# Performance work log

Hardware: AMD Instinct MI355X
Metric: run time of the kernel (lower is better)

Reference implementation:

```python
import jax, jax.numpy as jnp
import numpy as np

B, W, NN, EPG = 8, 16, 64, 1024   # batch, window, nodes/graph, trace-edges/graph
N = B * W * NN                     # 8192 flattened nodes
E = B * W * EPG                    # 131072 node-graph edges == trace rows
E2 = 4 * E                         # 524288 edge-graph (line-graph) edges
D_NODE = 128; D_LOG = 128; D_EDGE = 128
D_IN = D_NODE + D_LOG              # 256 = GATv2 node2node in_channels
H = 4
EPS = 1e-16                        # PyG softmax epsilon


def _lin(key, fan_in, fan_out):
    return jax.random.normal(key, (fan_in, fan_out), jnp.float32) * (1.0 / np.sqrt(fan_in))


def setup_inputs() -> dict:
    key = jax.random.key(0)
    ks = jax.random.split(key, 16)
    return {
        "x_node": jax.random.normal(ks[0], (B, W, NN, D_NODE), jnp.float32),
        "x_trace": jax.random.normal(ks[1], (B, W, EPG, D_EDGE), jnp.float32),
        "x_log": jax.random.normal(ks[2], (B, W, NN, D_LOG), jnp.float32),
        "node_adj": jax.random.randint(ks[3], (2, E), 0, N, jnp.int32),
        "edge_adj": jax.random.randint(ks[4], (2, E2), 0, E, jnp.int32),
        "edge_efea": jax.random.randint(ks[5], (E2,), 0, N, jnp.int32),
        # node2node GATv2Conv: in=256, heads=4, out/head=64, edge_dim=128
        "n2n_Wl": _lin(ks[6], D_IN, D_IN), "n2n_bl": jnp.zeros((D_IN,), jnp.float32),
        "n2n_Wr": _lin(ks[7], D_IN, D_IN), "n2n_br": jnp.zeros((D_IN,), jnp.float32),
        "n2n_We": _lin(ks[8], D_EDGE, D_IN),
        "n2n_att": jax.random.normal(ks[9], (H, D_IN // H), jnp.float32) * 0.1,
        "n2n_bias": jnp.zeros((D_IN,), jnp.float32),
        # egde2node GATv2Conv: in=128, heads=4, out/head=32, edge_dim=256
        "e2n_Wl": _lin(ks[10], D_EDGE, D_EDGE), "e2n_bl": jnp.zeros((D_EDGE,), jnp.float32),
        "e2n_Wr": _lin(ks[11], D_EDGE, D_EDGE), "e2n_br": jnp.zeros((D_EDGE,), jnp.float32),
        "e2n_We": _lin(ks[12], D_IN, D_EDGE),
        "e2n_att": jax.random.normal(ks[13], (H, D_EDGE // H), jnp.float32) * 0.1,
        "e2n_bias": jnp.zeros((D_EDGE,), jnp.float32),
    }


def gatv2(x, edge_index, edge_attr, Wl, bl, Wr, br, We, att, bias, num_nodes):
    """PyG GATv2Conv (eval mode, add_self_loops=False, concat heads)."""
    heads, C = att.shape
    src, dst = edge_index[0], edge_index[1]
    xl = (x @ Wl + bl).reshape(-1, heads, C)   # source transform [N,H,C]
    xr = (x @ Wr + br).reshape(-1, heads, C)   # target transform [N,H,C]
    e = (edge_attr @ We).reshape(-1, heads, C) # edge transform   [E,H,C]
    m = jax.nn.leaky_relu(xl[src] + xr[dst] + e, 0.2)  # [E,H,C]
    alpha = jnp.einsum('ehc,hc->eh', m, att)           # [E,H]
    amax = jax.ops.segment_max(alpha, dst, num_segments=num_nodes)
    ex = jnp.exp(alpha - amax[dst])
    denom = jax.ops.segment_sum(ex, dst, num_segments=num_nodes)
    a = ex / (denom[dst] + EPS)                        # per-target softmax
    out = jax.ops.segment_sum(a[:, :, None] * xl[src], dst, num_segments=num_nodes)
    return out.reshape(num_nodes, heads * C) + bias


def reference(x_node, x_trace, x_log, node_adj, edge_adj, edge_efea,
              n2n_Wl, n2n_bl, n2n_Wr, n2n_br, n2n_We, n2n_att, n2n_bias,
              e2n_Wl, e2n_bl, e2n_Wr, e2n_br, e2n_We, e2n_att, e2n_bias):
    node = jnp.concatenate([x_node, x_log], axis=-1).reshape(-1, D_IN)  # [N,256]
    trace = x_trace.reshape(-1, D_EDGE)                                 # [E,128]
    node = gatv2(node, node_adj, trace,
                 n2n_Wl, n2n_bl, n2n_Wr, n2n_br, n2n_We, n2n_att, n2n_bias, N)
    trace = gatv2(trace, edge_adj, node[edge_efea],
                  e2n_Wl, e2n_bl, e2n_Wr, e2n_br, e2n_We, e2n_att, e2n_bias, E)
    xn = node[:, :D_NODE].reshape(B, W, NN, D_NODE)
    xt = trace.reshape(B, W, EPG, D_EDGE)
    xlg = node[:, D_NODE:].reshape(B, W, NN, D_LOG)
    return (xn, xt, xlg)
```

## Files before the change

### kernel.cpp

```cpp
#include <hip/hip_runtime.h>
#include <hip/hip_bf16.h>

constexpr int N    = 8192;
constexpr int E    = 131072;
constexpr int E2   = 524288;

constexpr size_t XT_OFF  = (size_t)N * 128;
constexpr size_t XLG_OFF = XT_OFF + (size_t)E * 128;

typedef unsigned short u16;
typedef short s16x8 __attribute__((ext_vector_type(8)));
typedef float f32x4 __attribute__((ext_vector_type(4)));

__device__ __forceinline__ u16 f2bs(float f) {
    unsigned x = __float_as_uint(f);
    return (u16)((x + 0x7FFF + ((x >> 16) & 1)) >> 16);
}
__device__ __forceinline__ float bs2f(u16 u) {
    return __uint_as_float((unsigned)u << 16);
}

__global__ __launch_bounds__(256) void k_prep(
    const float* __restrict__ Wl, const float* __restrict__ Wr,
    const float* __restrict__ We, const float* __restrict__ Wl2,
    const float* __restrict__ Wr2, const float* __restrict__ We2,
    u16* __restrict__ Wlt, u16* __restrict__ Wrt, u16* __restrict__ Wet,
    u16* __restrict__ Wl2t, u16* __restrict__ Wr2t, u16* __restrict__ We2t)
{
    const int gid = blockIdx.x * 256 + threadIdx.x;
    const float* src; u16* dst; int base, Kk, sh;
    if      (gid <  65536) { src = Wl;  dst = Wlt;  base = 0;      Kk = 256; sh = 8; }
    else if (gid < 131072) { src = Wr;  dst = Wrt;  base = 65536;  Kk = 256; sh = 8; }
    else if (gid < 163840) { src = We;  dst = Wet;  base = 131072; Kk = 128; sh = 8; }
    else if (gid < 180224) { src = Wl2; dst = Wl2t; base = 163840; Kk = 128; sh = 7; }
    else if (gid < 196608) { src = Wr2; dst = Wr2t; base = 180224; Kk = 128; sh = 7; }
    else                   { src = We2; dst = We2t; base = 196608; Kk = 256; sh = 7; }
    const int l = gid - base;
    const int k = l >> sh, nn = l & ((1 << sh) - 1);
    dst[(size_t)nn * Kk + k] = f2bs(src[l]);
}

__global__ void k_hist(const int* __restrict__ dst, int* __restrict__ cnt, int nE)
{
    int i = blockIdx.x * 256 + threadIdx.x;
    if (i < nE) atomicAdd(&cnt[dst[i]], 1);
}

__global__ __launch_bounds__(1024) void k_scan(
    const int* __restrict__ cnt, int* __restrict__ off, int* __restrict__ cur, int n)
{
    __shared__ int tile[8192];
    __shared__ int wsum[16];
    const int tid = threadIdx.x, lane = tid & 63, wv = tid >> 6;
    int carry = 0;
    for (int base = 0; base < n; base += 8192) {
        for (int i = tid; i < 8192; i += 1024) tile[i] = cnt[base + i];
        __syncthreads();
        const int st = tid * 8;
        int s = 0;
        for (int k = 0; k < 8; ++k) { int v = tile[st + k]; tile[st + k] = s; s += v; }
        const int tsum = s;
        int incl = s;
        for (int o = 1; o < 64; o <<= 1) {
            int v = __shfl_up(incl, o);
            if (lane >= o) incl += v;
        }
        if (lane == 63) wsum[wv] = incl;
        __syncthreads();
        int woff = 0;
        for (int wq = 0; wq < wv; ++wq) woff += wsum[wq];
        int tot = 0;
        for (int wq = 0; wq < 16; ++wq) tot += wsum[wq];
        const int add = carry + woff + incl - tsum;
        for (int k = 0; k < 8; ++k) {
            int o2 = add + tile[st + k];
            off[base + st + k] = o2;
            cur[base + st + k] = o2;
        }
        carry += tot;
        __syncthreads();
    }
    if (tid == 0) off[n] = carry;
}

__global__ void k_scatter1(const int* __restrict__ adj, int* __restrict__ cur,
                           int* __restrict__ srcc, int* __restrict__ pos1, int nE)
{
    int i = blockIdx.x * 256 + threadIdx.x;
    if (i < nE) {
        int pos = atomicAdd(&cur[adj[nE + i]], 1);
        srcc[pos] = adj[i];
        pos1[i] = pos;
    }
}

__global__ void k_scatter2(const int* __restrict__ eadj, const int* __restrict__ efea,
                           int* __restrict__ cur, int2* __restrict__ sf2, int nE)
{
    int i = blockIdx.x * 256 + threadIdx.x;
    if (i < nE) {
        int pos = atomicAdd(&cur[eadj[nE + i]], 1);
        sf2[pos] = make_int2(eadj[i], efea[i]);
    }
}

__global__ __launch_bounds__(256) void k_node_gemm(
    const float* __restrict__ x_node, const float* __restrict__ x_log,
    const u16* __restrict__ Wlt, const float* __restrict__ bl,
    const u16* __restrict__ Wrt, const float* __restrict__ br,
    u16* __restrict__ xl, u16* __restrict__ xr)
{
    __shared__ u16 A[32][260];
    const int n0 = blockIdx.x * 32;
    const int tid = threadIdx.x;
    for (int i = tid; i < 32 * 64; i += 256) {
        const int r = i >> 6, k4 = (i & 63) << 2;
        const float* srcp = (k4 < 128) ? &x_node[(size_t)(n0 + r) * 128 + k4]
                                       : &x_log [(size_t)(n0 + r) * 128 + (k4 - 128)];
        const float4 v = *(const float4*)srcp;
        ushort4 o; o.x = f2bs(v.x); o.y = f2bs(v.y); o.z = f2bs(v.z); o.w = f2bs(v.w);
        *(ushort4*)&A[r][k4] = o;
    }
    __syncthreads();
    const int w = tid >> 6, lane = tid & 63, lr = lane & 15, lq = lane >> 4;
    const u16* Wt     = (w < 2) ? Wlt : Wrt;
    const float* bias = (w < 2) ? bl : br;
    u16* outp         = (w < 2) ? xl : xr;
    const int cb = (w & 1) * 128;
    f32x4 acc[2][8] = {};
    for (int kb = 0; kb < 8; ++kb) {
        s16x8 afr0 = *(const s16x8*)&A[lr][kb * 32 + lq * 8];
        s16x8 afr1 = *(const s16x8*)&A[16 + lr][kb * 32 + lq * 8];
#pragma unroll
        for (int ct = 0; ct < 8; ++ct) {
            const int n = cb + ct * 16 + lr;
            s16x8 bfr = *(const s16x8*)&Wt[(size_t)n * 256 + kb * 32 + lq * 8];
            acc[0][ct] = __builtin_amdgcn_mfma_f32_16x16x32_bf16(afr0, bfr, acc[0][ct], 0, 0, 0);
            acc[1][ct] = __builtin_amdgcn_mfma_f32_16x16x32_bf16(afr1, bfr, acc[1][ct], 0, 0, 0);
        }
    }
#pragma unroll
    for (int rt = 0; rt < 2; ++rt)
#pragma unroll
        for (int ct = 0; ct < 8; ++ct) {
            const int col = cb + ct * 16 + lr;
            const float bv = bias[col];
#pragma unroll
            for (int reg = 0; reg < 4; ++reg) {
                const int row = n0 + rt * 16 + lq * 4 + reg;
                outp[(size_t)row * 256 + col] = f2bs(acc[rt][ct][reg] + bv);
            }
        }
}

__global__ __launch_bounds__(256) void k_trace_gemm(
    const float* __restrict__ x_trace,
    const u16* __restrict__ Wl2t, const float* __restrict__ bl,
    const u16* __restrict__ Wr2t, const float* __restrict__ br,
    u16* __restrict__ xl, u16* __restrict__ xrst)
{
    __shared__ u16 A[32][132];
    const int e0 = blockIdx.x * 32;
    const int tid = threadIdx.x;
    for (int i = tid; i < 32 * 32; i += 256) {
        const int r = i >> 5, k4 = (i & 31) << 2;
        const float4 v = *(const float4*)&x_trace[(size_t)(e0 + r) * 128 + k4];
        ushort4 o; o.x = f2bs(v.x); o.y = f2bs(v.y); o.z = f2bs(v.z); o.w = f2bs(v.w);
        *(ushort4*)&A[r][k4] = o;
    }
    __syncthreads();
    const int w = tid >> 6, lane = tid & 63, lr = lane & 15, lq = lane >> 4;
    const u16* Wt     = (w < 2) ? Wl2t : Wr2t;
    const float* bias = (w < 2) ? bl : br;
    const int cb = (w & 1) * 64;
    f32x4 acc[2][4] = {};
    for (int kb = 0; kb < 4; ++kb) {
        s16x8 afr0 = *(const s16x8*)&A[lr][kb * 32 + lq * 8];
        s16x8 afr1 = *(const s16x8*)&A[16 + lr][kb * 32 + lq * 8];
#pragma unroll
        for (int ct = 0; ct < 4; ++ct) {
            const int n = cb + ct * 16 + lr;
            s16x8 bfr = *(const s16x8*)&Wt[(size_t)n * 128 + kb * 32 + lq * 8];
            acc[0][ct] = __builtin_amdgcn_mfma_f32_16x16x32_bf16(afr0, bfr, acc[0][ct], 0, 0, 0);
            acc[1][ct] = __builtin_amdgcn_mfma_f32_16x16x32_bf16(afr1, bfr, acc[1][ct], 0, 0, 0);
        }
    }
#pragma unroll
    for (int rt = 0; rt < 2; ++rt)
#pragma unroll
        for (int ct = 0; ct < 4; ++ct) {
            const int col = cb + ct * 16 + lr;
            const float bv = bias[col];
#pragma unroll
            for (int reg = 0; reg < 4; ++reg) {
                const int row = e0 + rt * 16 + lq * 4 + reg;
                if (w < 2) xl[(size_t)row * 128 + col]   = f2bs(acc[rt][ct][reg] + bv);
                else       xrst[(size_t)row * 256 + col] = f2bs(acc[rt][ct][reg] + bv);
            }
        }
}

__global__ __launch_bounds__(256) void k_edge_alpha1(
    const float* __restrict__ x_trace,
    const int* __restrict__ adj,
    const int* __restrict__ pos1,
    const u16* __restrict__ xl, const u16* __restrict__ xr,
    const u16* __restrict__ Wet, const float* __restrict__ att,
    float* __restrict__ alpha)
{
    __shared__ u16 A[32][132];
    __shared__ int ss[32], dd[32], pp[32];
    const int e0 = blockIdx.x * 32;
    const int tid = threadIdx.x;
    for (int i = tid; i < 32 * 32; i += 256) {
        const int r = i >> 5, k4 = (i & 31) << 2;
        const float4 v = *(const float4*)&x_trace[(size_t)(e0 + r) * 128 + k4];
        ushort4 o; o.x = f2bs(v.x); o.y = f2bs(v.y); o.z = f2bs(v.z); o.w = f2bs(v.w);
        *(ushort4*)&A[r][k4] = o;
    }
    if (tid < 32) {
        ss[tid] = adj[e0 + tid];
        dd[tid] = adj[E + e0 + tid];
        pp[tid] = pos1[e0 + tid];
    }
    __syncthreads();
    const int w = tid >> 6, lane = tid & 63, lr = lane & 15, lq = lane >> 4;
    f32x4 acc[2][4] = {};
    for (int kb = 0; kb < 4; ++kb) {
        s16x8 afr0 = *(const s16x8*)&A[lr][kb * 32 + lq * 8];
        s16x8 afr1 = *(const s16x8*)&A[16 + lr][kb * 32 + lq * 8];
#pragma unroll
        for (int ct = 0; ct < 4; ++ct) {
            const int n = w * 64 + ct * 16 + lr;
            s16x8 bfr = *(const s16x8*)&Wet[(size_t)n * 128 + kb * 32 + lq * 8];
            acc[0][ct] = __builtin_amdgcn_mfma_f32_16x16x32_bf16(afr0, bfr, acc[0][ct], 0, 0, 0);
            acc[1][ct] = __builtin_amdgcn_mfma_f32_16x16x32_bf16(afr1, bfr, acc[1][ct], 0, 0, 0);
        }
    }
    float attv[4];
#pragma unroll
    for (int ct = 0; ct < 4; ++ct) attv[ct] = att[w * 64 + ct * 16 + lr];
    float sums[2][4] = {};
#pragma unroll
    for (int rt = 0; rt < 2; ++rt)
#pragma unroll
        for (int reg = 0; reg < 4; ++reg) {
            const int rowt = rt * 16 + lq * 4 + reg;
            const int s = ss[rowt], d = dd[rowt];
            float acc_s = 0.f;
#pragma unroll
            for (int ct = 0; ct < 4; ++ct) {
                const int col = w * 64 + ct * 16 + lr;
                float m = acc[rt][ct][reg]
                        + bs2f(xl[(size_t)s * 256 + col])
                        + bs2f(xr[(size_t)d * 256 + col]);
                m = m > 0.f ? m : 0.2f * m;
                acc_s += m * attv[ct];
            }
            sums[rt][reg] = acc_s;
        }
#pragma unroll
    for (int rt = 0; rt < 2; ++rt)
#pragma unroll
        for (int reg = 0; reg < 4; ++reg) {
            float p = sums[rt][reg];
            p += __shfl_xor(p, 8);
            p += __shfl_xor(p, 4);
            p += __shfl_xor(p, 2);
            p += __shfl_xor(p, 1);
            if (lr == 0)
                alpha[(size_t)pp[rt * 16 + lq * 4 + reg] * 4 + w] = p;
        }
}

__global__ __launch_bounds__(256) void k_fused1(
    const int* __restrict__ off, const int* __restrict__ srcc,
    const float* __restrict__ alphac,
    const u16* __restrict__ xl,
    const float* __restrict__ bias,
    float* __restrict__ out)
{
    const int wv = __builtin_amdgcn_readfirstlane(threadIdx.x >> 6);
    const int lane = threadIdx.x & 63;
    const int n = blockIdx.x * 4 + wv;
    const int c = lane * 4;
    const int h = lane >> 4;
    const int beg = off[n], end = off[n + 1];
    float mx = -INFINITY, den = 0.f;
    float a0 = 0.f, a1 = 0.f, a2 = 0.f, a3 = 0.f;
    int i = beg;
    while (i < end) {
        const int rem = end - i;
        int sa[8]; float pe[8];
#pragma unroll
        for (int k = 0; k < 8; ++k) {
            const int idx = i + (k < rem ? k : rem - 1);
            sa[k] = srcc[idx];
            pe[k] = alphac[(size_t)idx * 4 + h];
        }
        ushort4 xv[8];
#pragma unroll
        for (int k = 0; k < 8; ++k)
            xv[k] = *(const ushort4*)&xl[(size_t)sa[k] * 256 + c];
#pragma unroll
        for (int k = 0; k < 8; ++k) {
            const float p = (k < rem) ? pe[k] : -INFINITY;
            const float mnew = fmaxf(mx, p);
            const float sc = __expf(mx - mnew);
            const float ex = __expf(p - mnew);
            den = den * sc + ex;
            a0 = a0 * sc + ex * bs2f(xv[k].x);
            a1 = a1 * sc + ex * bs2f(xv[k].y);
            a2 = a2 * sc + ex * bs2f(xv[k].z);
            a3 = a3 * sc + ex * bs2f(xv[k].w);
            mx = mnew;
        }
        i += 8;
    }
    const float inv = 1.f / (den + 1e-16f);
    float4 r;
    r.x = a0 * inv + bias[c + 0];
    r.y = a1 * inv + bias[c + 1];
    r.z = a2 * inv + bias[c + 2];
    r.w = a3 * inv + bias[c + 3];
    if (lane < 32) *(float4*)&out[(size_t)n * 128 + c] = r;
    else           *(float4*)&out[XLG_OFF + (size_t)n * 128 + (c - 128)] = r;
}

__global__ __launch_bounds__(256) void k_proj_gemm(
    const float* __restrict__ out_node, const u16* __restrict__ We2t,
    u16* __restrict__ proj)
{
    __shared__ u16 A[32][260];
    const int n0 = blockIdx.x * 32;
    const int tid = threadIdx.x;
    for (int i = tid; i < 32 * 64; i += 256) {
        const int r = i >> 6, k4 = (i & 63) << 2;
        const float* srcp = (k4 < 128)
            ? &out_node[(size_t)(n0 + r) * 128 + k4]
            : &out_node[XLG_OFF + (size_t)(n0 + r) * 128 + (k4 - 128)];
        const float4 v = *(const float4*)srcp;
        ushort4 o; o.x = f2bs(v.x); o.y = f2bs(v.y); o.z = f2bs(v.z); o.w = f2bs(v.w);
        *(ushort4*)&A[r][k4] = o;
    }
    __syncthreads();
    const int w = tid >> 6, lane = tid & 63, lr = lane & 15, lq = lane >> 4;
    f32x4 acc[2][2] = {};
    for (int kb = 0; kb < 8; ++kb) {
        s16x8 afr0 = *(const s16x8*)&A[lr][kb * 32 + lq * 8];
        s16x8 afr1 = *(const s16x8*)&A[16 + lr][kb * 32 + lq * 8];
#pragma unroll
        for (int ct = 0; ct < 2; ++ct) {
            const int col = w * 32 + ct * 16 + lr;
            s16x8 bfr = *(const s16x8*)&We2t[(size_t)col * 256 + kb * 32 + lq * 8];
            acc[0][ct] = __builtin_amdgcn_mfma_f32_16x16x32_bf16(afr0, bfr, acc[0][ct], 0, 0, 0);
            acc[1][ct] = __builtin_amdgcn_mfma_f32_16x16x32_bf16(afr1, bfr, acc[1][ct], 0, 0, 0);
        }
    }
#pragma unroll
    for (int rt = 0; rt < 2; ++rt)
#pragma unroll
        for (int ct = 0; ct < 2; ++ct) {
            const int col = w * 32 + ct * 16 + lr;
#pragma unroll
            for (int reg = 0; reg < 4; ++reg) {
                const int row = n0 + rt * 16 + lq * 4 + reg;
                proj[(size_t)row * 128 + col] = f2bs(acc[rt][ct][reg]);
            }
        }
}

__global__ __launch_bounds__(256) void k_fused2(
    const int* __restrict__ off, const int2* __restrict__ sf2,
    const u16* __restrict__ xl,
    const u16* __restrict__ proj,
    const float* __restrict__ att,
    const float* __restrict__ bias,
    float* __restrict__ out)
{
    const int wv = __builtin_amdgcn_readfirstlane(threadIdx.x >> 6);
    const int lane = threadIdx.x & 63;
    const int d = blockIdx.x * 4 + wv;
    const int c = lane * 2;
    const u16* xrst = (const u16*)(out + XT_OFF);
    const unsigned xrp = *(const unsigned*)&xrst[(size_t)d * 256 + c];
    const float xr0 = bs2f((u16)(xrp & 0xffff));
    const float xr1 = bs2f((u16)(xrp >> 16));
    const float av0 = att[c], av1 = att[c + 1];
    const int beg = off[d], end = off[d + 1];
    float mx = -INFINITY, den = 0.f, a0 = 0.f, a1 = 0.f;
    int i = beg;
    while (i < end) {
        const int rem = end - i;
        int2 sf[4];
#pragma unroll
        for (int k = 0; k < 4; ++k) sf[k] = sf2[i + (k < rem ? k : rem - 1)];
        unsigned xv[4], pv[4];
#pragma unroll
        for (int k = 0; k < 4; ++k) {
            xv[k] = *(const unsigned*)&xl[(size_t)sf[k].x * 128 + c];
            pv[k] = *(const unsigned*)&proj[(size_t)sf[k].y * 128 + c];
        }
#pragma unroll
        for (int k = 0; k < 4; ++k) {
            const float x0 = bs2f((u16)(xv[k] & 0xffff));
            const float x1 = bs2f((u16)(xv[k] >> 16));
            float m0 = x0 + xr0 + bs2f((u16)(pv[k] & 0xffff));
            float m1 = x1 + xr1 + bs2f((u16)(pv[k] >> 16));
            m0 = m0 > 0.f ? m0 : 0.2f * m0;
            m1 = m1 > 0.f ? m1 : 0.2f * m1;
            float pp = m0 * av0 + m1 * av1;
            pp += __shfl_xor(pp, 8, 16);
            pp += __shfl_xor(pp, 4, 16);
            pp += __shfl_xor(pp, 2, 16);
            pp += __shfl_xor(pp, 1, 16);
            const float p = (k < rem) ? pp : -INFINITY;
            const float mnew = fmaxf(mx, p);
            const float sc = __expf(mx - mnew);
            const float ex = __expf(p - mnew);
            den = den * sc + ex;
            a0 = a0 * sc + ex * x0;
            a1 = a1 * sc + ex * x1;
            mx = mnew;
        }
        i += 4;
    }
    const float inv = 1.f / (den + 1e-16f);
    float2 o2;
    o2.x = a0 * inv + bias[c];
    o2.y = a1 * inv + bias[c + 1];
    *(float2*)&out[XT_OFF + (size_t)d * 128 + c] = o2;
}

extern "C" void kernel_launch(void* const* d_in, const int* in_sizes, int n_in,
                              void* d_out, int out_size, void* d_ws, size_t ws_size,
                              hipStream_t stream)
{
    const float* x_node   = (const float*)d_in[0];
    const float* x_trace  = (const float*)d_in[1];
    const float* x_log    = (const float*)d_in[2];
    const int*   node_adj = (const int*)d_in[3];
    const int*   edge_adj = (const int*)d_in[4];
    const int*   efea     = (const int*)d_in[5];
    const float* n2n_Wl   = (const float*)d_in[6];
    const float* n2n_bl   = (const float*)d_in[7];
    const float* n2n_Wr   = (const float*)d_in[8];
    const float* n2n_br   = (const float*)d_in[9];
    const float* n2n_We   = (const float*)d_in[10];
    const float* n2n_att  = (const float*)d_in[11];
    const float* n2n_bias = (const float*)d_in[12];
    const float* e2n_Wl   = (const float*)d_in[13];
    const float* e2n_bl   = (const float*)d_in[14];
    const float* e2n_Wr   = (const float*)d_in[15];
    const float* e2n_br   = (const float*)d_in[16];
    const float* e2n_We   = (const float*)d_in[17];
    const float* e2n_att  = (const float*)d_in[18];
    const float* e2n_bias = (const float*)d_in[19];
    float* out = (float*)d_out;

    char* w = (char*)d_ws;
    int*  cnt1   = (int*)w;   w += (size_t)N * 4;
    int*  cnt2   = (int*)w;   w += (size_t)E * 4;
    int*  off1   = (int*)w;   w += (size_t)(N + 4) * 4;
    int*  cur1   = (int*)w;   w += (size_t)N * 4;
    int*  src1   = (int*)w;   w += (size_t)E * 4;
    int*  pos1   = (int*)w;   w += (size_t)E * 4;
    float* alphac = (float*)w; w += (size_t)E * 4 * 4;
    int*  off2   = (int*)w;   w += (size_t)(E + 4) * 4;
    int*  cur2   = (int*)w;   w += (size_t)E * 4;
    int2* sf2    = (int2*)w;  w += (size_t)E2 * 8;
    u16*  xl_n   = (u16*)w;   w += (size_t)N * 256 * 2;
    u16*  xr_n   = (u16*)w;   w += (size_t)N * 256 * 2;
    u16*  xl_e   = (u16*)w;   w += (size_t)E * 128 * 2;
    u16*  proj   = (u16*)w;   w += (size_t)N * 128 * 2;
    u16*  Wlt    = (u16*)w;   w += (size_t)65536 * 2;
    u16*  Wrt    = (u16*)w;   w += (size_t)65536 * 2;
    u16*  Wet    = (u16*)w;   w += (size_t)32768 * 2;
    u16*  Wl2t   = (u16*)w;   w += (size_t)16384 * 2;
    u16*  Wr2t   = (u16*)w;   w += (size_t)16384 * 2;
    u16*  We2t   = (u16*)w;   w += (size_t)32768 * 2;

    hipMemsetAsync(d_ws, 0, (size_t)(N + E) * 4, stream);

    k_prep<<<896, 256, 0, stream>>>(n2n_Wl, n2n_Wr, n2n_We, e2n_Wl, e2n_Wr, e2n_We,
                                    Wlt, Wrt, Wet, Wl2t, Wr2t, We2t);
    k_hist<<<E / 256, 256, 0, stream>>>(node_adj + E, cnt1, E);
    k_scan<<<1, 1024, 0, stream>>>(cnt1, off1, cur1, N);
    k_scatter1<<<E / 256, 256, 0, stream>>>(node_adj, cur1, src1, pos1, E);
    k_hist<<<E2 / 256, 256, 0, stream>>>(edge_adj + E2, cnt2, E2);
    k_scan<<<1, 1024, 0, stream>>>(cnt2, off2, cur2, E);
    k_scatter2<<<E2 / 256, 256, 0, stream>>>(edge_adj, efea, cur2, sf2, E2);

    k_node_gemm<<<N / 32, 256, 0, stream>>>(x_node, x_log, Wlt, n2n_bl, Wrt, n2n_br,
                                            xl_n, xr_n);
    k_edge_alpha1<<<E / 32, 256, 0, stream>>>(x_trace, node_adj, pos1, xl_n, xr_n,
                                              Wet, n2n_att, alphac);
    k_fused1<<<N / 4, 256, 0, stream>>>(off1, src1, alphac, xl_n, n2n_bias, out);

    k_proj_gemm<<<N / 32, 256, 0, stream>>>(out, We2t, proj);
    k_trace_gemm<<<E / 32, 256, 0, stream>>>(x_trace, Wl2t, e2n_bl, Wr2t, e2n_br,
                                             xl_e, (u16*)(out + XT_OFF));
    k_fused2<<<E / 4, 256, 0, stream>>>(off2, sf2, xl_e, proj,
                                        e2n_att, e2n_bias, out);
}
```

Baseline: 472.7 us.

## Fuse trace GEMM into edge-alpha kernel and permute weight columns for vector I/O

Merges the separate trace projection GEMM into the node-to-node edge attention kernel, so x_trace is read and converted to bf16 once and staged in LDS for both GEMMs. The weight transposition in the prep kernel now permutes output columns for We, Wl2 and Wr2. Each lane then holds four consecutive output columns, which lets the epilogue use ushort4 stores and ushort4 gathers of xl/xr instead of scalar accesses. The cost is more accumulator registers per thread, which may lower occupancy in the fused kernel.

```diff
diff --git a/kernel.cpp b/kernel.cpp
--- a/kernel.cpp
+++ b/kernel.cpp
@@ -28,16 +28,18 @@
     u16* __restrict__ Wl2t, u16* __restrict__ Wr2t, u16* __restrict__ We2t)
 {
     const int gid = blockIdx.x * 256 + threadIdx.x;
-    const float* src; u16* dst; int base, Kk, sh;
-    if      (gid <  65536) { src = Wl;  dst = Wlt;  base = 0;      Kk = 256; sh = 8; }
-    else if (gid < 131072) { src = Wr;  dst = Wrt;  base = 65536;  Kk = 256; sh = 8; }
-    else if (gid < 163840) { src = We;  dst = Wet;  base = 131072; Kk = 128; sh = 8; }
-    else if (gid < 180224) { src = Wl2; dst = Wl2t; base = 163840; Kk = 128; sh = 7; }
-    else if (gid < 196608) { src = Wr2; dst = Wr2t; base = 180224; Kk = 128; sh = 7; }
-    else                   { src = We2; dst = We2t; base = 196608; Kk = 256; sh = 7; }
+    const float* src; u16* dst; int base, Kk, sh, perm;
+    if      (gid <  65536) { src = Wl;  dst = Wlt;  base = 0;      Kk = 256; sh = 8; perm = 0; }
+    else if (gid < 131072) { src = Wr;  dst = Wrt;  base = 65536;  Kk = 256; sh = 8; perm = 0; }
+    else if (gid < 163840) { src = We;  dst = Wet;  base = 131072; Kk = 128; sh = 8; perm = 1; }
+    else if (gid < 180224) { src = Wl2; dst = Wl2t; base = 163840; Kk = 128; sh = 7; perm = 1; }
+    else if (gid < 196608) { src = Wr2; dst = Wr2t; base = 180224; Kk = 128; sh = 7; perm = 1; }
+    else                   { src = We2; dst = We2t; base = 196608; Kk = 256; sh = 7; perm = 0; }
     const int l = gid - base;
     const int k = l >> sh, nn = l & ((1 << sh) - 1);
-    dst[(size_t)nn * Kk + k] = f2bs(src[l]);
+    int ns = nn;
+    if (perm) ns = (nn & ~63) | ((nn & 3) << 4) | ((nn >> 2) & 15);
+    dst[(size_t)ns * Kk + k] = f2bs(src[l]);
 }
 
 __global__ void k_hist(const int* __restrict__ dst, int* __restrict__ cnt, int nE)
@@ -153,60 +155,16 @@
         }
 }
 
-__global__ __launch_bounds__(256) void k_trace_gemm(
-    const float* __restrict__ x_trace,
-    const u16* __restrict__ Wl2t, const float* __restrict__ bl,
-    const u16* __restrict__ Wr2t, const float* __restrict__ br,
-    u16* __restrict__ xl, u16* __restrict__ xrst)
-{
-    __shared__ u16 A[32][132];
-    const int e0 = blockIdx.x * 32;
-    const int tid = threadIdx.x;
-    for (int i = tid; i < 32 * 32; i += 256) {
-        const int r = i >> 5, k4 = (i & 31) << 2;
-        const float4 v = *(const float4*)&x_trace[(size_t)(e0 + r) * 128 + k4];
-        ushort4 o; o.x = f2bs(v.x); o.y = f2bs(v.y); o.z = f2bs(v.z); o.w = f2bs(v.w);
-        *(ushort4*)&A[r][k4] = o;
-    }
-    __syncthreads();
-    const int w = tid >> 6, lane = tid & 63, lr = lane & 15, lq = lane >> 4;
-    const u16* Wt     = (w < 2) ? Wl2t : Wr2t;
-    const float* bias = (w < 2) ? bl : br;
-    const int cb = (w & 1) * 64;
-    f32x4 acc[2][4] = {};
-    for (int kb = 0; kb < 4; ++kb) {
-        s16x8 afr0 = *(const s16x8*)&A[lr][kb * 32 + lq * 8];
-        s16x8 afr1 = *(const s16x8*)&A[16 + lr][kb * 32 + lq * 8];
-#pragma unroll
-        for (int ct = 0; ct < 4; ++ct) {
-            const int n = cb + ct * 16 + lr;
-            s16x8 bfr = *(const s16x8*)&Wt[(size_t)n * 128 + kb * 32 + lq * 8];
-            acc[0][ct] = __builtin_amdgcn_mfma_f32_16x16x32_bf16(afr0, bfr, acc[0][ct], 0, 0, 0);
-            acc[1][ct] = __builtin_amdgcn_mfma_f32_16x16x32_bf16(afr1, bfr, acc[1][ct], 0, 0, 0);
-        }
-    }
-#pragma unroll
-    for (int rt = 0; rt < 2; ++rt)
-#pragma unroll
-        for (int ct = 0; ct < 4; ++ct) {
-            const int col = cb + ct * 16 + lr;
-            const float bv = bias[col];
-#pragma unroll
-            for (int reg = 0; reg < 4; ++reg) {
-                const int row = e0 + rt * 16 + lq * 4 + reg;
-                if (w < 2) xl[(size_t)row * 128 + col]   = f2bs(acc[rt][ct][reg] + bv);
-                else       xrst[(size_t)row * 256 + col] = f2bs(acc[rt][ct][reg] + bv);
-            }
-        }
-}
-
-__global__ __launch_bounds__(256) void k_edge_alpha1(
+__global__ __launch_bounds__(256) void k_edge_mm(
     const float* __restrict__ x_trace,
     const int* __restrict__ adj,
     const int* __restrict__ pos1,
-    const u16* __restrict__ xl, const u16* __restrict__ xr,
-    const u16* __restrict__ Wet, const float* __restrict__ att,
-    float* __restrict__ alpha)
+    const u16* __restrict__ xl_n, const u16* __restrict__ xr_n,
+    const u16* __restrict__ Wet,
+    const u16* __restrict__ Wl2t, const float* __restrict__ bl2,
+    const u16* __restrict__ Wr2t, const float* __restrict__ br2,
+    const float* __restrict__ att,
+    float* __restrict__ alpha, u16* __restrict__ xl_e, u16* __restrict__ xrst)
 {
     __shared__ u16 A[32][132];
     __shared__ int ss[32], dd[32], pp[32];
@@ -225,40 +183,70 @@
     }
     __syncthreads();
     const int w = tid >> 6, lane = tid & 63, lr = lane & 15, lq = lane >> 4;
-    f32x4 acc[2][4] = {};
+    const u16* Wt2  = (w < 2) ? Wl2t : Wr2t;
+    const float* b2 = (w < 2) ? bl2 : br2;
+    const int cb2 = (w & 1) * 64;
+    f32x4 acc1[2][4] = {};
+    f32x4 acc2[2][4] = {};
     for (int kb = 0; kb < 4; ++kb) {
         s16x8 afr0 = *(const s16x8*)&A[lr][kb * 32 + lq * 8];
         s16x8 afr1 = *(const s16x8*)&A[16 + lr][kb * 32 + lq * 8];
 #pragma unroll
         for (int ct = 0; ct < 4; ++ct) {
-            const int n = w * 64 + ct * 16 + lr;
-            s16x8 bfr = *(const s16x8*)&Wet[(size_t)n * 128 + kb * 32 + lq * 8];
-            acc[0][ct] = __builtin_amdgcn_mfma_f32_16x16x32_bf16(afr0, bfr, acc[0][ct], 0, 0, 0);
-            acc[1][ct] = __builtin_amdgcn_mfma_f32_16x16x32_bf16(afr1, bfr, acc[1][ct], 0, 0, 0);
-        }
-    }
-    float attv[4];
-#pragma unroll
-    for (int ct = 0; ct < 4; ++ct) attv[ct] = att[w * 64 + ct * 16 + lr];
-    float sums[2][4] = {};
-#pragma unroll
-    for (int rt = 0; rt < 2; ++rt)
+            const int n1 = w * 64 + ct * 16 + lr;
+            s16x8 bfr = *(const s16x8*)&Wet[(size_t)n1 * 128 + kb * 32 + lq * 8];
+            acc1[0][ct] = __builtin_amdgcn_mfma_f32_16x16x32_bf16(afr0, bfr, acc1[0][ct], 0, 0, 0);
+            acc1[1][ct] = __builtin_amdgcn_mfma_f32_16x16x32_bf16(afr1, bfr, acc1[1][ct], 0, 0, 0);
+        }
+#pragma unroll
+        for (int ct = 0; ct < 4; ++ct) {
+            const int n2 = cb2 + ct * 16 + lr;
+            s16x8 bfr = *(const s16x8*)&Wt2[(size_t)n2 * 128 + kb * 32 + lq * 8];
+            acc2[0][ct] = __builtin_amdgcn_mfma_f32_16x16x32_bf16(afr0, bfr, acc2[0][ct], 0, 0, 0);
+            acc2[1][ct] = __builtin_amdgcn_mfma_f32_16x16x32_bf16(afr1, bfr, acc2[1][ct], 0, 0, 0);
+        }
+    }
+    {
+        const float4 b2q = *(const float4*)&b2[cb2 + lr * 4];
+#pragma unroll
+        for (int rt = 0; rt < 2; ++rt)
+#pragma unroll
+            for (int reg = 0; reg < 4; ++reg) {
+                const int row = e0 + rt * 16 + lq * 4 + reg;
+                ushort4 o;
+                o.x = f2bs(acc2[rt][0][reg] + b2q.x);
+                o.y = f2bs(acc2[rt][1][reg] + b2q.y);
+                o.z = f2bs(acc2[rt][2][reg] + b2q.z);
+                o.w = f2bs(acc2[rt][3][reg] + b2q.w);
+                if (w < 2) *(ushort4*)&xl_e[(size_t)row * 128 + cb2 + lr * 4] = o;
+                else       *(ushort4*)&xrst[(size_t)row * 256 + cb2 + lr * 4] = o;
+            }
+    }
+    const float4 attq = *(const float4*)&att[w * 64 + lr * 4];
+    const int co = w * 64 + lr * 4;
+    float sums[2][4];
+#pragma unroll
+    for (int rt = 0; rt < 2; ++rt) {
+        ushort4 xlv[4], xrv[4];
 #pragma unroll
         for (int reg = 0; reg < 4; ++reg) {
             const int rowt = rt * 16 + lq * 4 + reg;
-            const int s = ss[rowt], d = dd[rowt];
-            float acc_s = 0.f;
-#pragma unroll
-            for (int ct = 0; ct < 4; ++ct) {
-                const int col = w * 64 + ct * 16 + lr;
-                float m = acc[rt][ct][reg]
-                        + bs2f(xl[(size_t)s * 256 + col])
-                        + bs2f(xr[(size_t)d * 256 + col]);
-                m = m > 0.f ? m : 0.2f * m;
-                acc_s += m * attv[ct];
-            }
-            sums[rt][reg] = acc_s;
-        }
+            xlv[reg] = *(const ushort4*)&xl_n[(size_t)ss[rowt] * 256 + co];
+            xrv[reg] = *(const ushort4*)&xr_n[(size_t)dd[rowt] * 256 + co];
+        }
+#pragma unroll
+        for (int reg = 0; reg < 4; ++reg) {
+            float m0 = acc1[rt][0][reg] + bs2f(xlv[reg].x) + bs2f(xrv[reg].x);
+            float m1 = acc1[rt][1][reg] + bs2f(xlv[reg].y) + bs2f(xrv[reg].y);
+            float m2 = acc1[rt][2][reg] + bs2f(xlv[reg].z) + bs2f(xrv[reg].z);
+            float m3 = acc1[rt][3][reg] + bs2f(xlv[reg].w) + bs2f(xrv[reg].w);
+            m0 = m0 > 0.f ? m0 : 0.2f * m0;
+            m1 = m1 > 0.f ? m1 : 0.2f * m1;
+            m2 = m2 > 0.f ? m2 : 0.2f * m2;
+            m3 = m3 > 0.f ? m3 : 0.2f * m3;
+            sums[rt][reg] = m0 * attq.x + m1 * attq.y + m2 * attq.z + m3 * attq.w;
+        }
+    }
 #pragma unroll
     for (int rt = 0; rt < 2; ++rt)
 #pragma unroll
@@ -493,13 +481,12 @@
 
     k_node_gemm<<<N / 32, 256, 0, stream>>>(x_node, x_log, Wlt, n2n_bl, Wrt, n2n_br,
                                             xl_n, xr_n);
-    k_edge_alpha1<<<E / 32, 256, 0, stream>>>(x_trace, node_adj, pos1, xl_n, xr_n,
-                                              Wet, n2n_att, alphac);
+    k_edge_mm<<<E / 32, 256, 0, stream>>>(x_trace, node_adj, pos1, xl_n, xr_n,
+                                          Wet, Wl2t, e2n_bl, Wr2t, e2n_br,
+                                          n2n_att, alphac, xl_e, (u16*)(out + XT_OFF));
     k_fused1<<<N / 4, 256, 0, stream>>>(off1, src1, alphac, xl_n, n2n_bias, out);
 
     k_proj_gemm<<<N / 32, 256, 0, stream>>>(out, We2t, proj);
-    k_trace_gemm<<<E / 32, 256, 0, stream>>>(x_trace, Wl2t, e2n_bl, Wr2t, e2n_br,
-                                             xl_e, (u16*)(out + XT_OFF));
     k_fused2<<<E / 4, 256, 0, stream>>>(off2, sf2, xl_e, proj,
                                         e2n_att, e2n_bias, out);
 }
```

Result: no change. 469.4 us (-0.7%).
